# Kernel optimization log

Hardware: AMD Instinct MI355X
Metric: run time of the kernel (lower is better)

## Reference

```python
import jax, jax.numpy as jnp
import numpy as np

B, T, N, M, P, YD = 256, 64, 128, 256, 256, 1


def lstm_cell(x, h, c, Wih, Whh, bih, bhh):
    # torch LSTM gate order: i, f, g, o
    gates = x @ Wih.T + h @ Whh.T + bih + bhh  # (B, 4H)
    i, f, g, o = jnp.split(gates, 4, axis=-1)
    c_new = jax.nn.sigmoid(f) * c + jax.nn.sigmoid(i) * jnp.tanh(g)
    h_new = jax.nn.sigmoid(o) * jnp.tanh(c_new)
    return h_new, c_new


def setup_inputs() -> dict:
    key = jax.random.key(0)
    ks = jax.random.split(key, 20)
    s = 0.05
    return {
        "inputs": jax.random.normal(ks[0], (B, T, N + YD), jnp.float32),
        "WU_e": jax.random.normal(ks[1], (T, 2 * M + T), jnp.float32) * s,
        "v_e": jax.random.normal(ks[2], (1, T), jnp.float32) * s,
        "Wih_e": jax.random.normal(ks[3], (4 * M, N), jnp.float32) * s,
        "Whh_e": jax.random.normal(ks[4], (4 * M, M), jnp.float32) * s,
        "bih_e": jax.random.normal(ks[5], (4 * M,), jnp.float32) * s,
        "bhh_e": jax.random.normal(ks[6], (4 * M,), jnp.float32) * s,
        "WU_d": jax.random.normal(ks[7], (M, 2 * P + M), jnp.float32) * s,
        "v_d": jax.random.normal(ks[8], (1, M), jnp.float32) * s,
        "wb_tilde": jax.random.normal(ks[9], (1, YD + M), jnp.float32) * s,
        "Wih_d": jax.random.normal(ks[10], (4 * P, 1), jnp.float32) * s,
        "Whh_d": jax.random.normal(ks[11], (4 * P, P), jnp.float32) * s,
        "bih_d": jax.random.normal(ks[12], (4 * P,), jnp.float32) * s,
        "bhh_d": jax.random.normal(ks[13], (4 * P,), jnp.float32) * s,
        "Wb_W": jax.random.normal(ks[14], (P, P + M), jnp.float32) * s,
        "Wb_b": jax.random.normal(ks[15], (P,), jnp.float32) * s,
        "vb_W": jax.random.normal(ks[16], (YD, P), jnp.float32) * s,
        "vb_b": jax.random.normal(ks[17], (YD,), jnp.float32) * s,
    }


def _darnn(inputs, WU_e, v_e, Wih_e, Whh_e, bih_e, bhh_e,
           WU_d, v_d, wb_tilde, Wih_d, Whh_d, bih_d, bhh_d,
           Wb_W, Wb_b, vb_W, vb_b):
    X = inputs[:, :, :N]          # (B, T, N)
    Y = inputs[:, :, N:]          # (B, T, YD)
    X_nt = jnp.transpose(X, (0, 2, 1))  # (B, N, T), constant across encoder steps

    # ---------------- Encoder ----------------
    def enc_step(carry, x_t):  # x_t: (B, N)
        h, c = carry
        hs = jnp.concatenate([h, c], axis=-1)  # (B, 2M)
        feat = jnp.concatenate(
            [jnp.broadcast_to(hs[:, None, :], (B, N, 2 * M)), X_nt], axis=-1)  # (B, N, 2M+T)
        E = (jnp.tanh(feat @ WU_e.T) @ v_e.T)[..., 0]  # (B, N)
        alpha = jax.nn.softmax(E, axis=1)
        h, c = lstm_cell(x_t * alpha, h, c, Wih_e, Whh_e, bih_e, bhh_e)
        return (h, c), h

    h0 = jnp.zeros((B, M), inputs.dtype)
    c0 = jnp.zeros((B, M), inputs.dtype)
    _, X_encoded = jax.lax.scan(enc_step, (h0, c0), jnp.transpose(X, (1, 0, 2)))
    Xe_bm = jnp.transpose(X_encoded, (1, 0, 2))  # (B, T, M)

    # ---------------- Decoder ----------------
    def dec_step(carry, y_t):  # y_t: (B, YD)
        h, c, _ = carry
        hs = jnp.concatenate([h, c], axis=-1)  # (B, 2P)
        feat = jnp.concatenate(
            [jnp.broadcast_to(hs[:, None, :], (B, T, 2 * P)), Xe_bm], axis=-1)  # (B, T, 2P+M)
        l = (jnp.tanh(feat @ WU_d.T) @ v_d.T)[..., 0]  # (B, T)
        beta = jax.nn.softmax(l, axis=1)
        ctx = jnp.einsum('bt,btm->bm', beta, Xe_bm)  # (B, M)
        y_tilde = jnp.concatenate([y_t, ctx], axis=-1) @ wb_tilde.T  # (B, 1)
        h, c = lstm_cell(y_tilde, h, c, Wih_d, Whh_d, bih_d, bhh_d)
        return (h, c, ctx), None

    hd0 = jnp.zeros((B, P), inputs.dtype)
    cd0 = jnp.zeros((B, P), inputs.dtype)
    ctx0 = jnp.zeros((B, M), inputs.dtype)
    (h, c, ctx), _ = jax.lax.scan(
        dec_step, (hd0, cd0, ctx0), jnp.transpose(Y[:, :T - 1, :], (1, 0, 2)))

    hidden = jnp.concatenate([h, ctx], axis=-1) @ Wb_W.T + Wb_b  # (B, P)
    y_hat = hidden @ vb_W.T + vb_b  # (B, YD)
    return y_hat


def reference(inputs, WU_e, v_e, Wih_e, Whh_e, bih_e, bhh_e,
              WU_d, v_d, wb_tilde, Wih_d, Whh_d, bih_d, bhh_d,
              Wb_W, Wb_b, vb_W, vb_b):
    return _darnn(inputs, WU_e, v_e, Wih_e, Whh_e, bih_e, bhh_e,
                  WU_d, v_d, wb_tilde, Wih_d, Whh_d, bih_d, bhh_d,
                  Wb_W, Wb_b, vb_W, vb_b)
```

## Files before the change

### kernel.cpp

```cpp
#include <hip/hip_runtime.h>
#include <math.h>


#define OFF_XWT   0u
#define OFF_XEWT  2097152u
#define OFF_XE    6291456u
#define OFF_HE    10485760u
#define OFF_HD    10616832u
#define OFF_SB    10747904u
#define OFF_SDB   10780672u
#define OFF_XA    10911744u
#define OFF_CTX   10944512u
#define OFF_YT    11010048u
#define OFF_BAR   11010304u
#define WS_END    11010816u

#define SENT_U 0x7FC00001u

#define SLAB_F 24576
#define PER_F  2432
#define SCR_F  12288
#define FLG_F  16
#define SMEM_F (SLAB_F + PER_F + SCR_F + FLG_F)
#define SMEM_BYTES (SMEM_F * 4)

#define F_E 0
#define F_L 1
#define F_B 2
#define F_Y 3

__device__ __forceinline__ float fast_tanh(float x) {
  float xc = fminf(15.f, fmaxf(-15.f, x));
  float e = __expf(2.f * xc);
  return 1.f - 2.f * __builtin_amdgcn_rcpf(e + 1.f);
}
__device__ __forceinline__ float fast_sig(float x) {
  float xc = fminf(30.f, fmaxf(-30.f, x));
  return __builtin_amdgcn_rcpf(1.f + __expf(-xc));
}
__device__ __forceinline__ float wave_max(float v) {
#pragma unroll
  for (int o = 32; o; o >>= 1) v = fmaxf(v, __shfl_xor(v, o));
  return v;
}
__device__ __forceinline__ float wave_sum(float v) {
#pragma unroll
  for (int o = 32; o; o >>= 1) v += __shfl_xor(v, o);
  return v;
}
__device__ __forceinline__ float dot4(float4 a, float4 b) {
  return a.x*b.x + a.y*b.y + a.z*b.z + a.w*b.w;
}

__device__ __forceinline__ void st1_sc1(float* p, float v) {
  asm volatile("global_store_dword %0, %1, off sc1" :: "v"(p), "v"(v) : "memory");
}
__device__ __forceinline__ void ld1q_sc1(float4& a, const float* pa) {
  asm volatile("global_load_dwordx4 %0, %1, off sc1\n\ts_waitcnt vmcnt(0)"
               : "=&v"(a) : "v"(pa) : "memory");
}
__device__ __forceinline__ void ld1q_nw(float4& a, const float* pa) {
  asm volatile("global_load_dwordx4 %0, %1, off sc1"
               : "=&v"(a) : "v"(pa) : "memory");
}
__device__ __forceinline__ void vm0() {
  asm volatile("s_waitcnt vmcnt(0)" ::: "memory");
}
__device__ __forceinline__ void lgk0() {
  asm volatile("s_waitcnt lgkmcnt(0)" ::: "memory");
}
__device__ __forceinline__ float ld1s_sc1(const float* p) {
  float v;
  asm volatile("global_load_dword %0, %1, off sc1\n\ts_waitcnt vmcnt(0)"
               : "=&v"(v) : "v"(p) : "memory");
  return v;
}
__device__ __forceinline__ void ld8s_sc1(
    float& a0,float& a1,float& a2,float& a3,float& a4,float& a5,float& a6,float& a7,
    const float* p0,const float* p1,const float* p2,const float* p3,
    const float* p4,const float* p5,const float* p6,const float* p7) {
  asm volatile(
      "global_load_dword %0, %8, off sc1\n\t"
      "global_load_dword %1, %9, off sc1\n\t"
      "global_load_dword %2, %10, off sc1\n\t"
      "global_load_dword %3, %11, off sc1\n\t"
      "global_load_dword %4, %12, off sc1\n\t"
      "global_load_dword %5, %13, off sc1\n\t"
      "global_load_dword %6, %14, off sc1\n\t"
      "global_load_dword %7, %15, off sc1\n\t"
      "s_waitcnt vmcnt(0)"
      : "=&v"(a0),"=&v"(a1),"=&v"(a2),"=&v"(a3),
        "=&v"(a4),"=&v"(a5),"=&v"(a6),"=&v"(a7)
      : "v"(p0),"v"(p1),"v"(p2),"v"(p3),"v"(p4),"v"(p5),"v"(p6),"v"(p7)
      : "memory");
}
__device__ __forceinline__ void atomic_add_sc1(float* p, float v) {
  asm volatile("global_atomic_add_f32 %0, %1, off sc1" :: "v"(p), "v"(v) : "memory");
}

__device__ __forceinline__ void lds_inc(unsigned* f) {
  __hip_atomic_fetch_add(f, 1u, __ATOMIC_RELAXED, __HIP_MEMORY_SCOPE_WORKGROUP);
}
__device__ __forceinline__ void lds_poll(unsigned* f, unsigned tgt) {
  unsigned cur;
  do { cur = __hip_atomic_load(f, __ATOMIC_RELAXED, __HIP_MEMORY_SCOPE_WORKGROUP); } while (cur < tgt);
  asm volatile("" ::: "memory");
}

#define FMA16V(a0,a1,a2,a3,xv,wv) \
  a0.x += xv.x*wv.x; a0.y += xv.x*wv.y; a0.z += xv.x*wv.z; a0.w += xv.x*wv.w; \
  a1.x += xv.y*wv.x; a1.y += xv.y*wv.y; a1.z += xv.y*wv.z; a1.w += xv.y*wv.w; \
  a2.x += xv.z*wv.x; a2.y += xv.z*wv.y; a2.z += xv.z*wv.z; a2.w += xv.z*wv.w; \
  a3.x += xv.w*wv.x; a3.y += xv.w*wv.y; a3.z += xv.w*wv.z; a3.w += xv.w*wv.w;

__device__ __forceinline__ void bar_arrive(unsigned* bar) {
  asm volatile("s_waitcnt vmcnt(0)" ::: "memory");
  __syncthreads();
  if (threadIdx.x == 0)
    __hip_atomic_fetch_add(bar, 1u, __ATOMIC_RELAXED, __HIP_MEMORY_SCOPE_AGENT);
}
__device__ __forceinline__ void bar_wait(unsigned* bar, unsigned target) {
  if (threadIdx.x == 0) {
    unsigned cur;
    do {
      __builtin_amdgcn_s_sleep(1);
      cur = __hip_atomic_load(bar, __ATOMIC_RELAXED, __HIP_MEMORY_SCOPE_AGENT);
    } while (cur < target);
  }
  __syncthreads();
}

__global__ void darnn_init(float* __restrict__ ws, float* __restrict__ out) {
  unsigned i = blockIdx.x * 256u + threadIdx.x;
  const unsigned span = WS_END - OFF_HE;
  for (unsigned idx = i; idx < span; idx += gridDim.x * 256u) ws[OFF_HE + idx] = 0.f;
  if (i < 256u) out[i] = 0.f;
}

__global__ __launch_bounds__(512, 2) void darnn_main(
    const float* __restrict__ in,   const float* __restrict__ WUe,   const float* __restrict__ ve,
    const float* __restrict__ Wih_e,const float* __restrict__ Whh_e,
    const float* __restrict__ bih_e,const float* __restrict__ bhh_e,
    const float* __restrict__ WUd,  const float* __restrict__ vd,
    const float* __restrict__ wbt,  const float* __restrict__ Wih_d,
    const float* __restrict__ Whh_d,const float* __restrict__ bih_d, const float* __restrict__ bhh_d,
    const float* __restrict__ WbW,  const float* __restrict__ Wbb,
    const float* __restrict__ vbW,  const float* __restrict__ vbb,
    float* __restrict__ ws, float* __restrict__ out)
{
  extern __shared__ __align__(16) float sm[];
  float* SLAB = sm;
  float* PER  = sm + SLAB_F;
  float* SCR  = sm + SLAB_F + PER_F;
  unsigned* FLG = (unsigned*)(sm + SLAB_F + PER_F + SCR_F);
  const int tid = threadIdx.x;
  const int bid = blockIdx.x;
  const int grp = bid >> 4;
  const int mt  = bid & 15;
  const int b0  = grp << 4;
  const float SENTF = __uint_as_float(SENT_U);

  float* XWt  = ws + OFF_XWT;
  float* XeWt = ws + OFF_XEWT;
  float* Xe   = ws + OFF_XE;
  unsigned* barp = (unsigned*)(ws + OFF_BAR) + grp * 32;
  unsigned barn = 0;

  if (tid < FLG_F) FLG[tid] = 0u;

  float* wue_s  = PER;
  float* ve_s   = PER + 2304;
  float* bsum_e = PER + 2368;

  const int jfixE = ((tid & 63) + mt * 4) & 63;

  {
    int r = tid & 63, kq = tid >> 6;
    int grow = (r & 3) * 256 + mt * 16 + (r >> 2);
#pragma unroll 4
    for (int q = 0; q < 12; ++q) {
      int k = kq * 48 + q * 4;
      float4 wv = (k < 128) ? *(const float4*)(Wih_e + grow * 128 + k)
                            : *(const float4*)(Whh_e + grow * 256 + (k - 128));
      SLAB[(k + 0) * 64 + r] = wv.x; SLAB[(k + 1) * 64 + r] = wv.y;
      SLAB[(k + 2) * 64 + r] = wv.z; SLAB[(k + 3) * 64 + r] = wv.w;
    }
    {
      int lin = tid * 4;
      int j = lin >> 5, c0 = lin & 31;
      int col = (c0 < 16) ? (mt * 16 + c0) : (256 + mt * 16 + (c0 - 16));
      float4 wv = *(const float4*)(WUe + j * 576 + col);
      *(float4*)(wue_s + j * 36 + c0) = wv;
    }
    if (tid < 64) {
      ve_s[tid] = ve[tid];
      int g = tid >> 4, m2 = tid & 15, m = mt * 16 + m2;
      bsum_e[tid] = bih_e[g * 256 + m] + bhh_e[g * 256 + m];
    }
  }

  {
    float* Xs = SCR;
    const float* Xb = in + bid * 8256;
    __syncthreads();
    for (int it = 0; it < 16; ++it) {
      int lin = tid + it * 512;
      int k = lin >> 7, n = lin & 127;
      Xs[n * 68 + k] = Xb[k * 129 + n];
    }
    __syncthreads();
    int j = tid & 63, nh = tid >> 6;
    float acc[16];
#pragma unroll
    for (int i = 0; i < 16; ++i) acc[i] = 0.f;
    const float* wrow = WUe + j * 576 + 512;
    for (int kc = 0; kc < 4; ++kc) {
      float4 w0 = *(const float4*)(wrow + kc * 16 + 0);
      float4 w1 = *(const float4*)(wrow + kc * 16 + 4);
      float4 w2 = *(const float4*)(wrow + kc * 16 + 8);
      float4 w3 = *(const float4*)(wrow + kc * 16 + 12);
#pragma unroll
      for (int ni = 0; ni < 16; ++ni) {
        const float* xp = Xs + (nh * 16 + ni) * 68 + kc * 16;
        acc[ni] += dot4(*(const float4*)(xp + 0),  w0) + dot4(*(const float4*)(xp + 4),  w1)
                 + dot4(*(const float4*)(xp + 8),  w2) + dot4(*(const float4*)(xp + 12), w3);
      }
    }
    float* dst = XWt + bid * 8192 + j * 128 + nh * 16;
#pragma unroll
    for (int ni = 0; ni < 16; ++ni) dst[ni] = acc[ni];
    __syncthreads();
  }

  float4 whc[8];
#pragma unroll
  for (int q = 0; q < 8; ++q) whc[q] = *(const float4*)(wue_s + jfixE * 36 + q * 4);
  float4 bsE = {0,0,0,0};
  {
    int m2 = tid & 15;
    bsE.x = bsum_e[m2]; bsE.y = bsum_e[16 + m2];
    bsE.z = bsum_e[32 + m2]; bsE.w = bsum_e[48 + m2];
  }
  float xwreg[32];
  if (tid < 256) {
    int w = tid >> 6, l = tid & 63;
    const float* xwp = XWt + bid * 8192;
#pragma unroll
    for (int jj = 0; jj < 16; ++jj) {
      xwreg[jj]      = xwp[(w * 16 + jj) * 128 + l];
      xwreg[16 + jj] = xwp[(w * 16 + jj) * 128 + 64 + l];
    }
  }
  float c_reg = 0.f;

  for (int t = 0; t < 64; ++t) {
    const int rd = t & 1, wr2 = (t + 1) & 1;
    float* xah = SCR + 1024;
    const int ks = tid >> 6, ml = (tid >> 2) & 15, b4 = tid & 3;
    float4 a0 = {0,0,0,0}, a1 = {0,0,0,0}, a2 = {0,0,0,0}, a3 = {0,0,0,0};

    bar_wait(barp, barn);

    if (tid < 256) {
      int w = tid >> 6, l = tid & 63;
      float* Sj = SCR;
      float* Ep = SCR + 64;
      if (l < 16)
        Sj[w * 16 + l] = ld1s_sc1(ws + OFF_SB + (unsigned)rd * 16384 + (unsigned)bid * 64 + w * 16 + l);
      lgk0();
      float e0 = 0.f, e1 = 0.f;
#pragma unroll
      for (int jj = 0; jj < 16; ++jj) {
        float s = Sj[w * 16 + jj];
        float vv = ve_s[w * 16 + jj];
        e0 += vv * fast_tanh(xwreg[jj] + s);
        e1 += vv * fast_tanh(xwreg[16 + jj] + s);
      }
      Ep[w * 128 + l] = e0;
      Ep[w * 128 + 64 + l] = e1;
      lgk0();
      if (l == 0) lds_inc(FLG + F_E);
      if (w == 0) {
        lds_poll(FLG + F_E, 4u * (t + 1));
        float En0 = Ep[l] + Ep[128 + l] + Ep[256 + l] + Ep[384 + l];
        float En1 = Ep[64 + l] + Ep[192 + l] + Ep[320 + l] + Ep[448 + l];
        float mx = wave_max(fmaxf(En0, En1));
        float ex0 = __expf(En0 - mx), ex1 = __expf(En1 - mx);
        float tot = wave_sum(ex0 + ex1);
        float rt = __builtin_amdgcn_rcpf(tot);
        float x0 = in[bid * 8256 + t * 129 + l];
        float x1 = in[bid * 8256 + t * 129 + 64 + l];
        float* XAg = ws + OFF_XA + (unsigned)grp * 2048;
        st1_sc1(XAg + l * 16 + mt, x0 * ex0 * rt);
        st1_sc1(XAg + (64 + l) * 16 + mt, x1 * ex1 * rt);
        vm0();
        if (tid == 0)
          __hip_atomic_fetch_add(barp, 1u, __ATOMIC_RELAXED, __HIP_MEMORY_SCOPE_AGENT);
      }
    } else {
      int u = tid - 256;
      float4 h0, h1, h2, h3;
      const float* hb = ws + OFF_HE + (unsigned)rd * 65536 + (unsigned)grp * 4096 + u * 16;
      ld1q_nw(h0, hb); ld1q_nw(h1, hb + 4); ld1q_nw(h2, hb + 8); ld1q_nw(h3, hb + 12);
      vm0();
      float* row = xah + (unsigned)(128 + u) * 20;
      *(float4*)(row + 0) = h0; *(float4*)(row + 4) = h1;
      *(float4*)(row + 8) = h2; *(float4*)(row + 12) = h3;
      lgk0();
      int s = u >> 6;
      const float* xp = xah + (unsigned)(128 + s * 64) * 20 + b4 * 4;
      const float* wp = SLAB + (unsigned)(128 + s * 64) * 64 + ml * 4;
#pragma unroll 8
      for (int kk = 0; kk < 64; ++kk) {
        float4 xv = *(const float4*)(xp + kk * 20);
        float4 wv = *(const float4*)(wp + kk * 64);
        FMA16V(a0, a1, a2, a3, xv, wv);
      }
    }
    barn += 16;
    bar_wait(barp, barn);

    if (tid < 16) {
      float* sp = ws + OFF_SB + (unsigned)rd * 16384 + (unsigned)bid * 64 + tid * 4;
      float z01 = (t == 63 && tid == 0) ? SENTF : 0.f;
      st1_sc1(sp + 0, z01); st1_sc1(sp + 1, z01);
      st1_sc1(sp + 2, 0.f); st1_sc1(sp + 3, 0.f);
    }
    {
      int l = tid & 63;
      int k = (ks << 4) + (l >> 2), i4 = (l & 3) * 4;
      float4 q;
      ld1q_sc1(q, ws + OFF_XA + (unsigned)grp * 2048 + k * 16 + i4);
      *(float4*)(xah + k * 20 + i4) = q;
      lgk0();
    }
    {
      const float* xp = xah + (unsigned)(ks * 16) * 20 + b4 * 4;
      const float* wp = SLAB + (unsigned)(ks * 16) * 64 + ml * 4;
#pragma unroll 8
      for (int kk = 0; kk < 16; ++kk) {
        float4 xv = *(const float4*)(xp + kk * 20);
        float4 wv = *(const float4*)(wp + kk * 64);
        FMA16V(a0, a1, a2, a3, xv, wv);
      }
    }
    __syncthreads();
    float* red = SCR;
    {
      float* rp = red + (unsigned)(ks * 64 + ml * 4 + b4) * 20;
      *(float4*)(rp + 0) = a0; *(float4*)(rp + 4) = a1;
      *(float4*)(rp + 8) = a2; *(float4*)(rp + 12) = a3;
    }
    __syncthreads();
    float* hcs = SCR + 10240;
    if (tid < 256) {
      int m2 = tid & 15, bl = tid >> 4;
      int t2 = m2 * 4 + (bl >> 2), bs = bl & 3;
      float4 gate = {0,0,0,0};
#pragma unroll
      for (int k2 = 0; k2 < 8; ++k2) {
        float4 rr = *(const float4*)(red + (unsigned)(k2 * 64 + t2) * 20 + bs * 4);
        gate.x += rr.x; gate.y += rr.y; gate.z += rr.z; gate.w += rr.w;
      }
      float gi = gate.x + bsE.x, gf = gate.y + bsE.y;
      float gg = gate.z + bsE.z, go = gate.w + bsE.w;
      float cn = fast_sig(gf) * c_reg + fast_sig(gi) * fast_tanh(gg);
      float hn = fast_sig(go) * fast_tanh(cn);
      c_reg = cn;
      unsigned m = mt * 16 + m2;
      st1_sc1(ws + OFF_HE + (unsigned)wr2 * 65536 + (unsigned)grp * 4096 + m * 16 + bl, hn);
      st1_sc1(Xe + ((unsigned)(b0 + bl) * 64 + t) * 256 + m, hn);
      hcs[bl * 32 + m2] = hn;
      hcs[bl * 32 + 16 + m2] = cn;
    }
    __syncthreads();
    {
      int wq = tid >> 6;
#pragma unroll
      for (int e2 = 0; e2 < 2; ++e2) {
        int bl2 = wq * 2 + e2;
        const float* hp = hcs + bl2 * 32;
        float s = 0.f;
#pragma unroll
        for (int q = 0; q < 4; ++q) {
          s += dot4(*(const float4*)(hp + q * 4), whc[q]);
          s += dot4(*(const float4*)(hp + 16 + q * 4), whc[4 + q]);
        }
        atomic_add_sc1(ws + OFF_SB + (unsigned)wr2 * 16384 + (unsigned)(b0 + bl2) * 64 + jfixE, s);
      }
    }
    barn += 16;
    bar_arrive(barp);
  }
  bar_wait(barp, barn);

  float xe[64];
  if (tid < 256) {
    const float* xb = Xe + (unsigned)bid * 16384 + tid;
#pragma unroll
    for (int g8 = 0; g8 < 8; ++g8) {
      ld8s_sc1(xe[g8*8+0], xe[g8*8+1], xe[g8*8+2], xe[g8*8+3],
               xe[g8*8+4], xe[g8*8+5], xe[g8*8+6], xe[g8*8+7],
               xb + (g8*8+0)*256, xb + (g8*8+1)*256, xb + (g8*8+2)*256,
               xb + (g8*8+3)*256, xb + (g8*8+4)*256, xb + (g8*8+5)*256,
               xb + (g8*8+6)*256, xb + (g8*8+7)*256);
    }
  }

  float* vd_s   = PER;
  float* wbt_s  = PER + 256;
  float* bsum_d = PER + 520;
  float* wihd_s = PER + 584;
  float* wudT   = SLAB + 16384;
  const int jfixD = ((tid & 255) + mt * 16) & 255;
  __syncthreads();
  {
    int r = tid & 63, kq = tid >> 6;
    int grow = (r & 3) * 256 + mt * 16 + (r >> 2);
#pragma unroll 4
    for (int q = 0; q < 8; ++q) {
      int k = kq * 32 + q * 4;
      float4 wv = *(const float4*)(Whh_d + grow * 256 + k);
      SLAB[(k + 0) * 64 + r] = wv.x; SLAB[(k + 1) * 64 + r] = wv.y;
      SLAB[(k + 2) * 64 + r] = wv.z; SLAB[(k + 3) * 64 + r] = wv.w;
    }
    {
      int j = tid & 255, half = tid >> 8;
#pragma unroll
      for (int i = 0; i < 16; ++i) {
        int c = half * 16 + i;
        int col = (c < 16) ? (mt * 16 + c) : (256 + mt * 16 + (c - 16));
        wudT[c * 256 + j] = WUd[(unsigned)j * 768 + col];
      }
    }
    if (tid < 256) vd_s[tid] = vd[tid];
    if (tid < 257) wbt_s[tid] = wbt[tid];
    if (tid < 64) {
      int g = tid >> 4, m2 = tid & 15, m = mt * 16 + m2;
      bsum_d[tid] = bih_d[g * 256 + m] + bhh_d[g * 256 + m];
      wihd_s[tid] = Wih_d[g * 256 + m];
    }
  }
  __syncthreads();

  {
    float* XeT = SCR;
    float* Wdc = SCR + 4096;
    int tt2 = tid & 15, jq = tid >> 4;
    for (int jc = 0; jc < 2; ++jc) {
      float4 c0 = {0,0,0,0}, c1 = {0,0,0,0}, c2 = {0,0,0,0}, c3 = {0,0,0,0};
      for (int kc = 0; kc < 4; ++kc) {
        __syncthreads();
        if (tid < 256 && (tid >> 6) == kc) {
          int kk = tid & 63;
#pragma unroll
          for (int t4 = 0; t4 < 16; ++t4) {
            float4 v = { xe[t4*4+0], xe[t4*4+1], xe[t4*4+2], xe[t4*4+3] };
            *(float4*)(XeT + kk * 64 + t4 * 4) = v;
          }
        }
        {
          int jj = tid >> 2, k16 = (tid & 3) * 16;
          const float* src = WUd + (unsigned)(jc * 128 + jj) * 768 + 512 + kc * 64 + k16;
#pragma unroll
          for (int s4 = 0; s4 < 4; ++s4) {
            float4 wv = *(const float4*)(src + s4 * 4);
            Wdc[(k16 + s4*4 + 0) * 128 + jj] = wv.x;
            Wdc[(k16 + s4*4 + 1) * 128 + jj] = wv.y;
            Wdc[(k16 + s4*4 + 2) * 128 + jj] = wv.z;
            Wdc[(k16 + s4*4 + 3) * 128 + jj] = wv.w;
          }
        }
        __syncthreads();
#pragma unroll 8
        for (int kk = 0; kk < 64; ++kk) {
          float4 xv = *(const float4*)(XeT + kk * 64 + tt2 * 4);
          float4 wv = *(const float4*)(Wdc + kk * 128 + jq * 4);
          FMA16V(c0, c1, c2, c3, wv, xv);
        }
      }
      int jb = jc * 128 + jq * 4;
      *(float4*)(XeWt + ((unsigned)bid * 256 + jb + 0) * 64 + tt2 * 4) = c0;
      *(float4*)(XeWt + ((unsigned)bid * 256 + jb + 1) * 64 + tt2 * 4) = c1;
      *(float4*)(XeWt + ((unsigned)bid * 256 + jb + 2) * 64 + tt2 * 4) = c2;
      *(float4*)(XeWt + ((unsigned)bid * 256 + jb + 3) * 64 + tt2 * 4) = c3;
    }
    __syncthreads();
  }

  float wreg[32];
#pragma unroll
  for (int c = 0; c < 32; ++c) wreg[c] = wudT[c * 256 + jfixD];
  float4 bsD = {0,0,0,0}, wiD = {0,0,0,0};
  {
    int m2 = tid & 15;
    bsD.x = bsum_d[m2]; bsD.y = bsum_d[16 + m2]; bsD.z = bsum_d[32 + m2]; bsD.w = bsum_d[48 + m2];
    wiD.x = wihd_s[m2]; wiD.y = wihd_s[16 + m2]; wiD.z = wihd_s[32 + m2]; wiD.w = wihd_s[48 + m2];
  }
  float xewreg[64];
  if (tid < 256) {
    int w = tid >> 6, l = tid & 63;
    const float* xew = XeWt + (unsigned)bid * 16384 + l;
#pragma unroll
    for (int jj = 0; jj < 64; ++jj) xewreg[jj] = xew[(w * 64 + jj) << 6];
  }
  float cd_reg = 0.f;

  for (int t = 0; t < 63; ++t) {
    const int rd = t & 1, wr2 = (t + 1) & 1;
    const int ml = (tid >> 2) & 15, b4 = tid & 3;
    float* hT  = SCR + 2048;
    float* red = SCR + 7168;

    bar_wait(barp, barn);

    if (tid < 256) {
      int w = tid >> 6, l = tid & 63;
      float* Sdj  = SCR;
      float* lp   = SCR + 256;
      float* beta = SCR + 512;
      float* r8   = SCR + 576;
      Sdj[w * 64 + l] = ld1s_sc1(ws + OFF_SDB + (unsigned)rd * 65536 + (unsigned)bid * 256 + w * 64 + l);
      lgk0();
      float lpar = 0.f;
#pragma unroll 8
      for (int jj = 0; jj < 64; ++jj)
        lpar += vd_s[w * 64 + jj] * fast_tanh(xewreg[jj] + Sdj[w * 64 + jj]);
      lp[w * 64 + l] = lpar;
      lgk0();
      if (l == 0) lds_inc(FLG + F_L);
      if (w == 0) {
        lds_poll(FLG + F_L, 4u * (t + 1));
        float lv = lp[l] + lp[64 + l] + lp[128 + l] + lp[192 + l];
        float mx = wave_max(lv);
        float ex = __expf(lv - mx);
        float sw = wave_sum(ex);
        beta[l] = ex * __builtin_amdgcn_rcpf(sw);
        lgk0();
        if (l == 0) lds_inc(FLG + F_B);
      }
      lds_poll(FLG + F_B, (unsigned)(t + 1));
      lgk0();
      float ctx = 0.f;
#pragma unroll
      for (int tt = 0; tt < 64; ++tt) ctx += beta[tt] * xe[tt];
      if (t == 62)
        st1_sc1(ws + OFF_CTX + (unsigned)bid * 256 + tid, ctx);
      float yp = ctx * wbt_s[1 + tid];
      float swv = wave_sum(yp);
      if (l == 0) r8[w] = swv;
      lgk0();
      if (l == 0) lds_inc(FLG + F_Y);
      if (w == 0) {
        lds_poll(FLG + F_Y, 4u * (t + 1));
        if (l == 0) {
          float yt = wbt_s[0] * in[bid * 8256 + t * 129 + 128] + r8[0] + r8[1] + r8[2] + r8[3];
          st1_sc1(ws + OFF_SB + 16384u + (unsigned)bid * 64u + (unsigned)rd, yt);
        }
      }
    } else {
      if (tid == 256)
        st1_sc1(ws + OFF_SB + 16384u + (unsigned)bid * 64u + (unsigned)wr2, SENTF);
      int u = tid - 256;
      float4 h0, h1, h2, h3;
      const float* hb = ws + OFF_HD + (unsigned)rd * 65536 + (unsigned)grp * 4096 + u * 16;
      ld1q_nw(h0, hb); ld1q_nw(h1, hb + 4); ld1q_nw(h2, hb + 8); ld1q_nw(h3, hb + 12);
      vm0();
      float* row = hT + (unsigned)u * 20;
      *(float4*)(row + 0) = h0; *(float4*)(row + 4) = h1;
      *(float4*)(row + 8) = h2; *(float4*)(row + 12) = h3;
      lgk0();
      int s = u >> 6;
      float4 a0 = {0,0,0,0}, a1 = {0,0,0,0}, a2 = {0,0,0,0}, a3 = {0,0,0,0};
      const float* xp = hT + (unsigned)(s * 64) * 20 + b4 * 4;
      const float* wp = SLAB + (unsigned)(s * 64) * 64 + ml * 4;
#pragma unroll 8
      for (int kk = 0; kk < 64; ++kk) {
        float4 xv = *(const float4*)(xp + kk * 20);
        float4 wv = *(const float4*)(wp + kk * 64);
        FMA16V(a0, a1, a2, a3, xv, wv);
      }
      float* rp = red + (unsigned)(s * 64 + ml * 4 + b4) * 20;
      *(float4*)(rp + 0) = a0; *(float4*)(rp + 4) = a1;
      *(float4*)(rp + 8) = a2; *(float4*)(rp + 12) = a3;
    }
    if (tid < 64) {
      float* sp = ws + OFF_SDB + (unsigned)rd * 65536 + (unsigned)bid * 256 + tid * 4;
      st1_sc1(sp + 0, 0.f); st1_sc1(sp + 1, 0.f);
      st1_sc1(sp + 2, 0.f); st1_sc1(sp + 3, 0.f);
    }
    __syncthreads();

    float* hcs = SCR;
    if (tid < 256) {
      int m2 = tid & 15, bl = tid >> 4;
      int t2 = m2 * 4 + (bl >> 2), bs = bl & 3;
      float4 gate = {0,0,0,0};
#pragma unroll
      for (int k2 = 0; k2 < 4; ++k2) {
        float4 rr = *(const float4*)(red + (unsigned)(k2 * 64 + t2) * 20 + bs * 4);
        gate.x += rr.x; gate.y += rr.y; gate.z += rr.z; gate.w += rr.w;
      }
      const float* pyt = ws + OFF_SB + 16384u + (unsigned)(b0 + bl) * 64u + (unsigned)rd;
      float yt_reg = ld1s_sc1(pyt);
      while (__float_as_uint(yt_reg) == SENT_U) {
        __builtin_amdgcn_s_sleep(1);
        yt_reg = ld1s_sc1(pyt);
      }
      float gi = gate.x + yt_reg * wiD.x + bsD.x;
      float gf = gate.y + yt_reg * wiD.y + bsD.y;
      float gg = gate.z + yt_reg * wiD.z + bsD.z;
      float go = gate.w + yt_reg * wiD.w + bsD.w;
      float cn = fast_sig(gf) * cd_reg + fast_sig(gi) * fast_tanh(gg);
      float hn = fast_sig(go) * fast_tanh(cn);
      cd_reg = cn;
      unsigned m = mt * 16 + m2;
      st1_sc1(ws + OFF_HD + (unsigned)wr2 * 65536 + (unsigned)grp * 4096 + m * 16 + bl, hn);
      hcs[bl * 32 + m2] = hn;
      hcs[bl * 32 + 16 + m2] = cn;
    }
    __syncthreads();
    {
      int half = tid >> 8;
#pragma unroll
      for (int e2 = 0; e2 < 8; ++e2) {
        int bl2 = half * 8 + e2;
        const float* hp = hcs + bl2 * 32;
        float s = 0.f;
#pragma unroll
        for (int c = 0; c < 16; ++c) s += hp[c] * wreg[c];
#pragma unroll
        for (int c = 0; c < 16; ++c) s += hp[16 + c] * wreg[16 + c];
        atomic_add_sc1(ws + OFF_SDB + (unsigned)wr2 * 65536 + (unsigned)(b0 + bl2) * 256 + jfixD, s);
      }
    }
    barn += 16;
    bar_arrive(barp);
  }
  bar_wait(barp, barn);

  {
    float* hsf  = SCR;
    float* hid2 = SCR + 8256;
    {
      int l0 = tid * 2, l1 = tid * 2 + 1;
      int k0 = l0 >> 2, i0 = l0 & 3, k1 = l1 >> 2, i1 = l1 & 3;
      const float* hb = ws + OFF_HD + 65536u + (unsigned)grp * 4096;
      int bl0 = l0 >> 6, c0 = (l0 & 63) * 4, bl1 = l1 >> 6, c1 = (l1 & 63) * 4;
      float4 qa, qb, qc, qd;
      ld1q_nw(qa, hb + k0 * 16 + i0 * 4);
      ld1q_nw(qb, hb + k1 * 16 + i1 * 4);
      ld1q_nw(qc, ws + OFF_CTX + (unsigned)(b0 + bl0) * 256 + c0);
      ld1q_nw(qd, ws + OFF_CTX + (unsigned)(b0 + bl1) * 256 + c1);
      vm0();
      hsf[(i0 * 4 + 0) * 516 + k0] = qa.x; hsf[(i0 * 4 + 1) * 516 + k0] = qa.y;
      hsf[(i0 * 4 + 2) * 516 + k0] = qa.z; hsf[(i0 * 4 + 3) * 516 + k0] = qa.w;
      hsf[(i1 * 4 + 0) * 516 + k1] = qb.x; hsf[(i1 * 4 + 1) * 516 + k1] = qb.y;
      hsf[(i1 * 4 + 2) * 516 + k1] = qb.z; hsf[(i1 * 4 + 3) * 516 + k1] = qb.w;
      *(float4*)(hsf + bl0 * 516 + 256 + c0) = qc;
      *(float4*)(hsf + bl1 * 516 + 256 + c1) = qd;
    }
    __syncthreads();
    int bl = tid & 15, p4 = (tid >> 4) & 15, half = tid >> 8;
    int row = mt * 16 + p4;
    const float* wrow = WbW + (unsigned)row * 512 + half * 256;
    const float* hp = hsf + bl * 516 + half * 256;
    float acc = half ? 0.f : Wbb[row];
#pragma unroll 8
    for (int q = 0; q < 64; ++q)
      acc += dot4(*(const float4*)(hp + q * 4), *(const float4*)(wrow + q * 4));
    hid2[half * 272 + bl * 17 + p4] = acc;
    __syncthreads();
    if (tid < 16) {
      float s = 0.f;
#pragma unroll
      for (int p = 0; p < 16; ++p)
        s += (hid2[tid * 17 + p] + hid2[272 + tid * 17 + p]) * vbW[mt * 16 + p];
      if (mt == 0) s += vbb[0];
      atomicAdd(&out[b0 + tid], s);
    }
  }
}

extern "C" void kernel_launch(void* const* d_in, const int* in_sizes, int n_in,
                              void* d_out, int out_size, void* d_ws, size_t ws_size,
                              hipStream_t stream) {
  (void)in_sizes; (void)n_in; (void)out_size; (void)ws_size;
  const float* in    = (const float*)d_in[0];
  const float* WUe   = (const float*)d_in[1];
  const float* ve    = (const float*)d_in[2];
  const float* Wih_e = (const float*)d_in[3];
  const float* Whh_e = (const float*)d_in[4];
  const float* bih_e = (const float*)d_in[5];
  const float* bhh_e = (const float*)d_in[6];
  const float* WUd   = (const float*)d_in[7];
  const float* vd    = (const float*)d_in[8];
  const float* wbt   = (const float*)d_in[9];
  const float* Wih_d = (const float*)d_in[10];
  const float* Whh_d = (const float*)d_in[11];
  const float* bih_d = (const float*)d_in[12];
  const float* bhh_d = (const float*)d_in[13];
  const float* WbW   = (const float*)d_in[14];
  const float* Wbb   = (const float*)d_in[15];
  const float* vbW   = (const float*)d_in[16];
  const float* vbb   = (const float*)d_in[17];
  float* ws  = (float*)d_ws;
  float* out = (float*)d_out;

  (void)hipFuncSetAttribute((const void*)darnn_main,
                            hipFuncAttributeMaxDynamicSharedMemorySize, SMEM_BYTES);
  hipLaunchKernelGGL(darnn_init, dim3(1024), dim3(256), 0, stream, ws, out);
  hipLaunchKernelGGL(darnn_main, dim3(256), dim3(512), SMEM_BYTES, stream,
                     in, WUe, ve, Wih_e, Whh_e, bih_e, bhh_e,
                     WUd, vd, wbt, Wih_d, Whh_d, bih_d, bhh_d,
                     WbW, Wbb, vbW, vbb, ws, out);
}
```

Measured before the change: 1.283 ms.

## Precompute wbt·Xe projection so y_tilde skips per-step context reduction

Uses linearity: y_tilde = w0*y + sum_t beta_t * (wbt·Xe_t), so q_t = wbt·Xe_t is precomputed once per batch row before the decoder loop. Each step then needs only one wave reduction of exp*q scaled by the softmax reciprocal. This removes the per-step beta broadcast, the 64-term context dot product, a second wave_sum and two LDS flag sync rounds. The full context is now computed only on the final step; the y inputs are preloaded into registers, and the sentinel spin sleep is lengthened, which may add wake-up latency.

```diff
diff --git a/kernel.cpp b/kernel.cpp
--- a/kernel.cpp
+++ b/kernel.cpp
@@ -27,7 +27,6 @@
 #define F_E 0
 #define F_L 1
 #define F_B 2
-#define F_Y 3
 
 __device__ __forceinline__ float fast_tanh(float x) {
   float xc = fminf(15.f, fmaxf(-15.f, x));
@@ -411,6 +410,8 @@
   float* wbt_s  = PER + 256;
   float* bsum_d = PER + 520;
   float* wihd_s = PER + 584;
+  float* q_s    = PER + 704;
+  float* qpart  = PER + 768;
   float* wudT   = SLAB + 16384;
   const int jfixD = ((tid & 255) + mt * 16) & 255;
   __syncthreads();
@@ -441,6 +442,19 @@
       wihd_s[tid] = Wih_d[g * 256 + m];
     }
   }
+  __syncthreads();
+
+  if (tid < 256) {
+    int w = tid >> 6, l = tid & 63;
+    float wm = wbt_s[1 + tid];
+#pragma unroll
+    for (int t4 = 0; t4 < 64; ++t4) {
+      float v = wave_sum(wm * xe[t4]);
+      if (l == 0) qpart[w * 64 + t4] = v;
+    }
+  }
+  __syncthreads();
+  if (tid < 64) q_s[tid] = qpart[tid] + qpart[64 + tid] + qpart[128 + tid] + qpart[192 + tid];
   __syncthreads();
 
   {
@@ -504,6 +518,12 @@
 #pragma unroll
     for (int jj = 0; jj < 64; ++jj) xewreg[jj] = xew[(w * 64 + jj) << 6];
   }
+  float q_reg = 0.f, yv = 0.f;
+  if (tid < 64) {
+    q_reg = q_s[tid];
+    if (tid < 63) yv = in[bid * 8256 + tid * 129 + 128];
+  }
+  const float wbt0 = wbt_s[0];
   float cd_reg = 0.f;
 
   for (int t = 0; t < 63; ++t) {
@@ -519,7 +539,6 @@
       float* Sdj  = SCR;
       float* lp   = SCR + 256;
       float* beta = SCR + 512;
-      float* r8   = SCR + 576;
       Sdj[w * 64 + l] = ld1s_sc1(ws + OFF_SDB + (unsigned)rd * 65536 + (unsigned)bid * 256 + w * 64 + l);
       lgk0();
       float lpar = 0.f;
@@ -535,28 +554,25 @@
         float mx = wave_max(lv);
         float ex = __expf(lv - mx);
         float sw = wave_sum(ex);
-        beta[l] = ex * __builtin_amdgcn_rcpf(sw);
-        lgk0();
-        if (l == 0) lds_inc(FLG + F_B);
-      }
-      lds_poll(FLG + F_B, (unsigned)(t + 1));
-      lgk0();
-      float ctx = 0.f;
-#pragma unroll
-      for (int tt = 0; tt < 64; ++tt) ctx += beta[tt] * xe[tt];
-      if (t == 62)
-        st1_sc1(ws + OFF_CTX + (unsigned)bid * 256 + tid, ctx);
-      float yp = ctx * wbt_s[1 + tid];
-      float swv = wave_sum(yp);
-      if (l == 0) r8[w] = swv;
-      lgk0();
-      if (l == 0) lds_inc(FLG + F_Y);
-      if (w == 0) {
-        lds_poll(FLG + F_Y, 4u * (t + 1));
+        float rt = __builtin_amdgcn_rcpf(sw);
+        float ytn = wave_sum(ex * q_reg);
         if (l == 0) {
-          float yt = wbt_s[0] * in[bid * 8256 + t * 129 + 128] + r8[0] + r8[1] + r8[2] + r8[3];
+          float yt = wbt0 * __shfl(yv, t) + ytn * rt;
           st1_sc1(ws + OFF_SB + 16384u + (unsigned)bid * 64u + (unsigned)rd, yt);
         }
+        if (t == 62) {
+          beta[l] = ex * rt;
+          lgk0();
+          if (l == 0) lds_inc(FLG + F_B);
+        }
+      }
+      if (t == 62) {
+        lds_poll(FLG + F_B, 1u);
+        lgk0();
+        float ctx = 0.f;
+#pragma unroll
+        for (int tt = 0; tt < 64; ++tt) ctx += beta[tt] * xe[tt];
+        st1_sc1(ws + OFF_CTX + (unsigned)bid * 256 + tid, ctx);
       }
     } else {
       if (tid == 256)
@@ -604,7 +620,7 @@
       const float* pyt = ws + OFF_SB + 16384u + (unsigned)(b0 + bl) * 64u + (unsigned)rd;
       float yt_reg = ld1s_sc1(pyt);
       while (__float_as_uint(yt_reg) == SENT_U) {
-        __builtin_amdgcn_s_sleep(1);
+        __builtin_amdgcn_s_sleep(4);
         yt_reg = ld1s_sc1(pyt);
       }
       float gi = gate.x + yt_reg * wiD.x + bsD.x;
```

After: 1.241 ms. -3.3%, faster.
